# Kernel optimization log

Measured on AMD Instinct MI355X. Metric: run time of the kernel, lower is better.

## Reference

```python
import jax, jax.numpy as jnp
import numpy as np
from jax import lax

B, IN, H, OUT, M, R = 16384, 512, 1024, 512, 8, 256


def setup_inputs() -> dict:
    key = jax.random.key(0)
    ks = jax.random.split(key, 14)
    s = lambda *sh: 1.0 / np.sqrt(sh[-2] if len(sh) > 1 else sh[-1])
    return {
        "x": jax.random.normal(ks[0], (B, IN), jnp.float32),
        "W_in": jax.random.normal(ks[1], (IN, H), jnp.float32) * (1.0 / np.sqrt(IN)),
        "b_in": jnp.zeros((H,), jnp.float32),
        "W_mod": jax.random.normal(ks[2], (M, H, H), jnp.float32) * (1.0 / np.sqrt(H)),
        "b_mod": jnp.zeros((M, H), jnp.float32),
        "Wr1": jax.random.normal(ks[3], (H, R), jnp.float32) * (1.0 / np.sqrt(H)),
        "br1": jnp.zeros((R,), jnp.float32),
        "Wr2": jax.random.normal(ks[4], (R, M), jnp.float32) * (1.0 / np.sqrt(R)),
        "br2": jnp.zeros((M,), jnp.float32),
        "Wc": jax.random.normal(ks[5], (1, H), jnp.float32),
        "bc": jnp.zeros((H,), jnp.float32),
        "W_out": jax.random.normal(ks[6], (H, OUT), jnp.float32) * (1.0 / np.sqrt(H)),
        "b_out": jnp.zeros((OUT,), jnp.float32),
        "max_cycles": 4,
    }


def reference(x, W_in, b_in, W_mod, b_mod, Wr1, br1, Wr2, br2, Wc, bc, W_out, b_out, max_cycles):
    h = x @ W_in + b_in                      # [B, H]
    orig = h

    def body(h, c):
        # cycle_projection: Linear(1, H) applied to scalar cycle index c
        cycle_proj = c * Wc[0] + bc          # [H]
        r = jax.nn.relu((orig * cycle_proj) @ Wr1 + br1)   # [B, R]
        probs = jax.nn.softmax(r @ Wr2 + br2, axis=-1)     # [B, M]
        # all experts as one batched GEMM: [B,H] x [M,H,H] -> [B,M,H]
        expert = jax.nn.relu(jnp.einsum('bh,mhd->bmd', h, W_mod) + b_mod)
        h_new = jnp.einsum('bmd,bm->bd', expert, probs)    # softmax-weighted sum
        return h_new, None

    h, _ = lax.scan(body, h, jnp.arange(max_cycles, dtype=x.dtype))
    return h @ W_out + b_out                 # [B, OUT]
```

## Files before the change

### kernel.cpp

```cpp
#include <hip/hip_runtime.h>


typedef _Float16 half8 __attribute__((ext_vector_type(8)));
typedef _Float16 half4v __attribute__((ext_vector_type(4)));
typedef float floatx4 __attribute__((ext_vector_type(4)));

#define DEVI __device__ __forceinline__

DEVI void async16(void* lds, const void* g) {
  __builtin_amdgcn_global_load_lds(
      (const __attribute__((address_space(1))) unsigned int*)g,
      (__attribute__((address_space(3))) unsigned int*)lds, 16, 0, 0);
}

DEVI floatx4 mfma_f16(half8 a, half8 b, floatx4 c) {
  return __builtin_amdgcn_mfma_f32_16x16x32_f16(a, b, c, 0, 0, 0);
}


__global__ __launch_bounds__(256) void k_cast16(const float* __restrict__ in,
                                                _Float16* __restrict__ o,
                                                int n4) {
  int i = blockIdx.x * 256 + threadIdx.x;
  if (i >= n4) return;
  float4 v = ((const float4*)in)[i];
  half4v h;
  h[0] = (_Float16)v.x;
  h[1] = (_Float16)v.y;
  h[2] = (_Float16)v.z;
  h[3] = (_Float16)v.w;
  ((half4v*)o)[i] = h;
}

__global__ __launch_bounds__(256) void k_transpose16(
    const float* __restrict__ in, const float* __restrict__ scale,
    _Float16* __restrict__ o, int R, int C) {
  __shared__ float tile[64][65];
  __shared__ float srow[64];
  int b = blockIdx.z;
  int r0 = blockIdx.y * 64, c0 = blockIdx.x * 64;
  const float* src = in + (size_t)b * R * C;
  int t = threadIdx.x;
  int lr = t >> 4;
  int lc4 = (t & 15) * 4;
#pragma unroll
  for (int rr = 0; rr < 64; rr += 16) {
    float4 v = *(const float4*)&src[(size_t)(r0 + lr + rr) * C + c0 + lc4];
    tile[lr + rr][lc4 + 0] = v.x;
    tile[lr + rr][lc4 + 1] = v.y;
    tile[lr + rr][lc4 + 2] = v.z;
    tile[lr + rr][lc4 + 3] = v.w;
  }
  if (t < 64) srow[t] = scale ? scale[r0 + t] : 1.0f;
  __syncthreads();
  int oc = t >> 2;
  int orr = (t & 3) * 16;
  alignas(16) _Float16 hv[16];
#pragma unroll
  for (int k = 0; k < 16; k++)
    hv[k] = (_Float16)(tile[orr + k][oc] * srow[orr + k]);
  size_t ob = (size_t)b * C * R + (size_t)(c0 + oc) * R + (r0 + orr);
  ((int4*)&o[ob])[0] = ((int4*)hv)[0];
  ((int4*)&o[ob])[1] = ((int4*)hv)[1];
}


__global__ __launch_bounds__(256) void k_gemm_f16(
    const _Float16* __restrict__ A, const _Float16* __restrict__ Bt,
    const float* __restrict__ bias, _Float16* __restrict__ O, int M, int N,
    int K) {
  __shared__ _Float16 sA[128 * 32], sB[128 * 32];
  int t = threadIdx.x, lane = t & 63, wave = t >> 6;
  int wr = wave >> 1, wc = wave & 1;
  int row0 = blockIdx.y * 128, col0 = blockIdx.x * 128;
  floatx4 acc[4][4];
  for (int i = 0; i < 4; i++)
    for (int j = 0; j < 4; j++) acc[i][j] = (floatx4){0.f, 0.f, 0.f, 0.f};
  int rr0 = t >> 2, kk0 = (t & 3) * 8;
  int ar = (lane & 15) * 32 + (lane >> 4) * 8;
  for (int k0 = 0; k0 < K; k0 += 32) {
    __syncthreads();
    async16(&sA[t * 8], &A[(size_t)(row0 + rr0) * K + k0 + kk0]);
    async16(&sA[(t + 256) * 8], &A[(size_t)(row0 + rr0 + 64) * K + k0 + kk0]);
    async16(&sB[t * 8], &Bt[(size_t)(col0 + rr0) * K + k0 + kk0]);
    async16(&sB[(t + 256) * 8], &Bt[(size_t)(col0 + rr0 + 64) * K + k0 + kk0]);
    __syncthreads();
    half8 a[4], b[4];
#pragma unroll
    for (int i = 0; i < 4; i++) {
      a[i] = *(const half8*)&sA[(wr * 64 + i * 16) * 32 + ar];
      b[i] = *(const half8*)&sB[(wc * 64 + i * 16) * 32 + ar];
    }
#pragma unroll
    for (int i = 0; i < 4; i++)
#pragma unroll
      for (int j = 0; j < 4; j++) acc[i][j] = mfma_f16(a[i], b[j], acc[i][j]);
  }
#pragma unroll
  for (int i = 0; i < 4; i++) {
    int rowb = row0 + wr * 64 + i * 16 + ((lane >> 4) << 2);
#pragma unroll
    for (int j = 0; j < 4; j++) {
      int col = col0 + wc * 64 + j * 16 + (lane & 15);
      float bv = bias ? bias[col] : 0.0f;
#pragma unroll
      for (int r = 0; r < 4; r++)
        O[(size_t)(rowb + r) * N + col] = (_Float16)(acc[i][j][r] + bv);
    }
  }
}

__global__ __launch_bounds__(256) void k_gemm_f32(
    const _Float16* __restrict__ A, const _Float16* __restrict__ Bt,
    const float* __restrict__ bias, float* __restrict__ O, int M, int N,
    int K) {
  __shared__ _Float16 sA[128 * 32], sB[128 * 32];
  int t = threadIdx.x, lane = t & 63, wave = t >> 6;
  int wr = wave >> 1, wc = wave & 1;
  int row0 = blockIdx.y * 128, col0 = blockIdx.x * 128;
  floatx4 acc[4][4];
  for (int i = 0; i < 4; i++)
    for (int j = 0; j < 4; j++) acc[i][j] = (floatx4){0.f, 0.f, 0.f, 0.f};
  int rr0 = t >> 2, kk0 = (t & 3) * 8;
  int ar = (lane & 15) * 32 + (lane >> 4) * 8;
  for (int k0 = 0; k0 < K; k0 += 32) {
    __syncthreads();
    async16(&sA[t * 8], &A[(size_t)(row0 + rr0) * K + k0 + kk0]);
    async16(&sA[(t + 256) * 8], &A[(size_t)(row0 + rr0 + 64) * K + k0 + kk0]);
    async16(&sB[t * 8], &Bt[(size_t)(col0 + rr0) * K + k0 + kk0]);
    async16(&sB[(t + 256) * 8], &Bt[(size_t)(col0 + rr0 + 64) * K + k0 + kk0]);
    __syncthreads();
    half8 a[4], b[4];
#pragma unroll
    for (int i = 0; i < 4; i++) {
      a[i] = *(const half8*)&sA[(wr * 64 + i * 16) * 32 + ar];
      b[i] = *(const half8*)&sB[(wc * 64 + i * 16) * 32 + ar];
    }
#pragma unroll
    for (int i = 0; i < 4; i++)
#pragma unroll
      for (int j = 0; j < 4; j++) acc[i][j] = mfma_f16(a[i], b[j], acc[i][j]);
  }
#pragma unroll
  for (int i = 0; i < 4; i++) {
    int rowb = row0 + wr * 64 + i * 16 + ((lane >> 4) << 2);
#pragma unroll
    for (int j = 0; j < 4; j++) {
      int col = col0 + wc * 64 + j * 16 + (lane & 15);
      float bv = bias ? bias[col] : 0.0f;
#pragma unroll
      for (int r = 0; r < 4; r++)
        O[(size_t)(rowb + r) * N + col] = acc[i][j][r] + bv;
    }
  }
}


__global__ __launch_bounds__(256) void k_router4(
    const float* __restrict__ PQ, const float* __restrict__ br1,
    const float* __restrict__ Wr2, const float* __restrict__ br2,
    float* __restrict__ probs, int B) {
  int lane = threadIdx.x & 63;
  int wave = threadIdx.x >> 6;
  int row = blockIdx.x * 4 + wave;
  float cval = (float)blockIdx.y;
  float4 p4 = ((const float4*)(PQ + (size_t)row * 512))[lane];
  float4 q4 = ((const float4*)(PQ + (size_t)row * 512 + 256))[lane];
  float4 b4 = ((const float4*)br1)[lane];
  float rv[4];
  rv[0] = fmaxf(cval * p4.x + q4.x + b4.x, 0.f);
  rv[1] = fmaxf(cval * p4.y + q4.y + b4.y, 0.f);
  rv[2] = fmaxf(cval * p4.z + q4.z + b4.z, 0.f);
  rv[3] = fmaxf(cval * p4.w + q4.w + b4.w, 0.f);
  float lg[8] = {0.f, 0.f, 0.f, 0.f, 0.f, 0.f, 0.f, 0.f};
#pragma unroll
  for (int k = 0; k < 4; k++) {
    const float4* w = (const float4*)(Wr2 + (size_t)(lane * 4 + k) * 8);
    float4 w0 = w[0], w1 = w[1];
    lg[0] += rv[k] * w0.x;
    lg[1] += rv[k] * w0.y;
    lg[2] += rv[k] * w0.z;
    lg[3] += rv[k] * w0.w;
    lg[4] += rv[k] * w1.x;
    lg[5] += rv[k] * w1.y;
    lg[6] += rv[k] * w1.z;
    lg[7] += rv[k] * w1.w;
  }
#pragma unroll
  for (int s = 32; s > 0; s >>= 1)
#pragma unroll
    for (int m = 0; m < 8; m++) lg[m] += __shfl_xor(lg[m], s);
#pragma unroll
  for (int m = 0; m < 8; m++) lg[m] += br2[m];
  float mx = lg[0];
#pragma unroll
  for (int m = 1; m < 8; m++) mx = fmaxf(mx, lg[m]);
  float e[8];
  float sum = 0.f;
#pragma unroll
  for (int m = 0; m < 8; m++) {
    e[m] = expf(lg[m] - mx);
    sum += e[m];
  }
  float inv = 1.f / sum;
  if (lane < 8)
    probs[(size_t)blockIdx.y * B * 8 + (size_t)row * 8 + lane] = e[lane] * inv;
}


__global__ __launch_bounds__(256) void k_expert_partial(
    const _Float16* __restrict__ hin, const _Float16* __restrict__ WT,
    const float* __restrict__ bmod, const float* __restrict__ probs,
    _Float16* __restrict__ part, int rowbase) {
  __shared__ _Float16 sA[128 * 32];
  __shared__ _Float16 sB[128 * 32];
  __shared__ float sProb[128];
  __shared__ float sBias[128];
  const int K = 1024;
  int t = threadIdx.x, lane = t & 63, wave = t >> 6;
  int wr = wave >> 1, wc = wave & 1;
  int m = blockIdx.z;
  int col0 = blockIdx.x * 128;
  int prow0 = blockIdx.y * 128;
  int grow0 = rowbase + prow0;
  if (t < 128)
    sProb[t] = probs[(size_t)(grow0 + t) * 8 + m];
  else
    sBias[t - 128] = bmod[(size_t)m * 1024 + col0 + (t - 128)];
  const _Float16* Bm = WT + (size_t)m * 1024 * 1024;
  floatx4 acc[4][4];
  for (int i = 0; i < 4; i++)
    for (int j = 0; j < 4; j++) acc[i][j] = (floatx4){0.f, 0.f, 0.f, 0.f};
  int rr0 = t >> 2, kk0 = (t & 3) * 8;
  int ar = (lane & 15) * 32 + (lane >> 4) * 8;
  for (int k0 = 0; k0 < K; k0 += 32) {
    __syncthreads();
    async16(&sA[t * 8], &hin[(size_t)(grow0 + rr0) * K + k0 + kk0]);
    async16(&sA[(t + 256) * 8],
            &hin[(size_t)(grow0 + rr0 + 64) * K + k0 + kk0]);
    async16(&sB[t * 8], &Bm[(size_t)(col0 + rr0) * K + k0 + kk0]);
    async16(&sB[(t + 256) * 8], &Bm[(size_t)(col0 + rr0 + 64) * K + k0 + kk0]);
    __syncthreads();
    half8 a[4], b[4];
#pragma unroll
    for (int i = 0; i < 4; i++) {
      a[i] = *(const half8*)&sA[(wr * 64 + i * 16) * 32 + ar];
      b[i] = *(const half8*)&sB[(wc * 64 + i * 16) * 32 + ar];
    }
#pragma unroll
    for (int i = 0; i < 4; i++)
#pragma unroll
      for (int j = 0; j < 4; j++) acc[i][j] = mfma_f16(a[i], b[j], acc[i][j]);
  }
#pragma unroll
  for (int i = 0; i < 4; i++) {
    int lr0 = wr * 64 + i * 16 + ((lane >> 4) << 2);
    float p0 = sProb[lr0 + 0];
    float p1 = sProb[lr0 + 1];
    float p2 = sProb[lr0 + 2];
    float p3 = sProb[lr0 + 3];
#pragma unroll
    for (int j = 0; j < 4; j++) {
      int cl = wc * 64 + j * 16 + (lane & 15);
      float bb = sBias[cl];
      size_t base =
          (size_t)m * 4096 * 1024 + (size_t)(prow0 + lr0) * 1024 + col0 + cl;
      part[base + 0 * 1024] = (_Float16)(p0 * fmaxf(acc[i][j][0] + bb, 0.f));
      part[base + 1 * 1024] = (_Float16)(p1 * fmaxf(acc[i][j][1] + bb, 0.f));
      part[base + 2 * 1024] = (_Float16)(p2 * fmaxf(acc[i][j][2] + bb, 0.f));
      part[base + 3 * 1024] = (_Float16)(p3 * fmaxf(acc[i][j][3] + bb, 0.f));
    }
  }
}

__global__ __launch_bounds__(256) void k_combine8(
    const _Float16* __restrict__ part, _Float16* __restrict__ hout,
    int rowbase) {
  const size_t S = (size_t)4096 * 1024;
  size_t i = ((size_t)blockIdx.x * 256 + threadIdx.x) * 8;
  float s[8] = {0.f, 0.f, 0.f, 0.f, 0.f, 0.f, 0.f, 0.f};
#pragma unroll
  for (int m = 0; m < 8; m++) {
    half8 v = *(const half8*)&part[(size_t)m * S + i];
#pragma unroll
    for (int k = 0; k < 8; k++) s[k] += (float)v[k];
  }
  half8 o;
#pragma unroll
  for (int k = 0; k < 8; k++) o[k] = (_Float16)s[k];
  *(half8*)&hout[(size_t)rowbase * 1024 + i] = o;
}


extern "C" void kernel_launch(void* const* d_in, const int* in_sizes, int n_in,
                              void* d_out, int out_size, void* d_ws,
                              size_t ws_size, hipStream_t stream) {
  (void)in_sizes;
  (void)n_in;
  (void)out_size;
  (void)ws_size;
  const float* x = (const float*)d_in[0];
  const float* W_in = (const float*)d_in[1];
  const float* b_in = (const float*)d_in[2];
  const float* W_mod = (const float*)d_in[3];
  const float* b_mod = (const float*)d_in[4];
  const float* Wr1 = (const float*)d_in[5];
  const float* br1 = (const float*)d_in[6];
  const float* Wr2 = (const float*)d_in[7];
  const float* br2 = (const float*)d_in[8];
  const float* Wc = (const float*)d_in[9];
  const float* bc = (const float*)d_in[10];
  const float* W_out = (const float*)d_in[11];
  const float* b_out = (const float*)d_in[12];
  float* out = (float*)d_out;

  const int B = 16384, IN = 512, H = 1024, OUT = 512, M = 8, R = 256;
  const size_t MB = 1024 * 1024;

  char* p = (char*)d_ws;
  _Float16* partial = (_Float16*)(p + 0);
  _Float16* xh = (_Float16*)(p + 0);
  _Float16* WinT = (_Float16*)(p + 64 * MB);
  _Float16* W1T = (_Float16*)(p + 65 * MB);
  _Float16* WoutT = (_Float16*)(p + 66 * MB);
  _Float16* WmodT = (_Float16*)(p + 67 * MB);
  _Float16* origHi = (_Float16*)(p + 83 * MB);
  _Float16* hA = (_Float16*)(p + 115 * MB);
  _Float16* hB = (_Float16*)(p + 147 * MB);
  float* PQ = (float*)(p + 179 * MB);
  float* probs4 = (float*)(p + 211 * MB);

  k_cast16<<<dim3(B * IN / 4 / 256), dim3(256), 0, stream>>>(x, xh,
                                                             B * IN / 4);
  k_transpose16<<<dim3(H / 64, IN / 64, 1), dim3(256), 0, stream>>>(
      W_in, nullptr, WinT, IN, H);
  k_transpose16<<<dim3(R / 64, H / 64, 1), dim3(256), 0, stream>>>(
      Wr1, Wc, W1T, H, R);
  k_transpose16<<<dim3(R / 64, H / 64, 1), dim3(256), 0, stream>>>(
      Wr1, bc, W1T + (size_t)R * H, H, R);
  k_transpose16<<<dim3(OUT / 64, H / 64, 1), dim3(256), 0, stream>>>(
      W_out, nullptr, WoutT, H, OUT);
  k_transpose16<<<dim3(H / 64, H / 64, M), dim3(256), 0, stream>>>(
      W_mod, nullptr, WmodT, H, H);

  k_gemm_f16<<<dim3(H / 128, B / 128), dim3(256), 0, stream>>>(
      xh, WinT, b_in, origHi, B, H, IN);
  k_gemm_f32<<<dim3(2 * R / 128, B / 128), dim3(256), 0, stream>>>(
      origHi, W1T, nullptr, PQ, B, 2 * R, H);
  k_router4<<<dim3(B / 4, 4), dim3(256), 0, stream>>>(PQ, br1, Wr2, br2,
                                                      probs4, B);

  const _Float16* hcur = origHi;
  _Float16* hbufs[2] = {hA, hB};
  for (int c = 0; c < 4; c++) {
    const float* probs = probs4 + (size_t)c * B * 8;
    _Float16* hn = hbufs[c & 1];
    for (int chunk = 0; chunk < 4; chunk++) {
      int rowbase = chunk * 4096;
      k_expert_partial<<<dim3(H / 128, 32, M), dim3(256), 0, stream>>>(
          hcur, WmodT, b_mod, probs, partial, rowbase);
      k_combine8<<<dim3(4096 * 1024 / (256 * 8)), dim3(256), 0, stream>>>(
          partial, hn, rowbase);
    }
    hcur = hn;
  }

  k_gemm_f32<<<dim3(OUT / 128, B / 128), dim3(256), 0, stream>>>(
      hcur, WoutT, b_out, out, B, OUT, H);
}
```

Baseline: 1.907 ms.

## Compute expert pairs per block, summing them before writing halved partials

Each block now covers a 256-row tile and two experts (z and z+4) at once. The A tile is loaded once and shared across both experts, and their prob-weighted ReLU outputs are added in registers before one fp16 partial is stored. This halves the partial-buffer writes and the combine reads, and lets the row chunk grow to 8192 with fewer launches. The cost is doubled accumulator register use per thread (512-thread blocks with launch bounds of 2) and more LDS, which may lower occupancy.

```diff
diff --git a/kernel.cpp b/kernel.cpp
--- a/kernel.cpp
+++ b/kernel.cpp
@@ -6,6 +6,7 @@
 typedef float floatx4 __attribute__((ext_vector_type(4)));
 
 #define DEVI __device__ __forceinline__
+#define CHUNK 8192
 
 DEVI void async16(void* lds, const void* g) {
   __builtin_amdgcn_global_load_lds(
@@ -208,79 +209,99 @@
 }
 
 
-__global__ __launch_bounds__(256) void k_expert_partial(
+__global__ __launch_bounds__(512, 2) void k_expert_pair(
     const _Float16* __restrict__ hin, const _Float16* __restrict__ WT,
     const float* __restrict__ bmod, const float* __restrict__ probs,
     _Float16* __restrict__ part, int rowbase) {
-  __shared__ _Float16 sA[128 * 32];
-  __shared__ _Float16 sB[128 * 32];
-  __shared__ float sProb[128];
-  __shared__ float sBias[128];
+  __shared__ _Float16 sA[256 * 32];
+  __shared__ _Float16 sB[2 * 128 * 32];
+  __shared__ float sProb[2 * 256];
+  __shared__ float sBias[2 * 128];
   const int K = 1024;
   int t = threadIdx.x, lane = t & 63, wave = t >> 6;
-  int wr = wave >> 1, wc = wave & 1;
-  int m = blockIdx.z;
+  int wr = wave >> 1;
+  int wc = wave & 1;
+  int z = blockIdx.z;
   int col0 = blockIdx.x * 128;
-  int prow0 = blockIdx.y * 128;
+  int prow0 = blockIdx.y * 256;
   int grow0 = rowbase + prow0;
-  if (t < 128)
-    sProb[t] = probs[(size_t)(grow0 + t) * 8 + m];
-  else
-    sBias[t - 128] = bmod[(size_t)m * 1024 + col0 + (t - 128)];
-  const _Float16* Bm = WT + (size_t)m * 1024 * 1024;
-  floatx4 acc[4][4];
+  if (t < 512) {
+    int e = t >> 8, r = t & 255;
+    sProb[t] = probs[(size_t)(grow0 + r) * 8 + z + e * 4];
+  }
+  if (t < 256) {
+    int e = t >> 7, cc = t & 127;
+    sBias[t] = bmod[(size_t)(z + e * 4) * 1024 + col0 + cc];
+  }
+  const _Float16* B0 = WT + (size_t)z * 1024 * 1024;
+  const _Float16* B1 = WT + (size_t)(z + 4) * 1024 * 1024;
+  floatx4 acc0[4][4], acc1[4][4];
+#pragma unroll
   for (int i = 0; i < 4; i++)
-    for (int j = 0; j < 4; j++) acc[i][j] = (floatx4){0.f, 0.f, 0.f, 0.f};
+#pragma unroll
+    for (int j = 0; j < 4; j++) {
+      acc0[i][j] = (floatx4){0.f, 0.f, 0.f, 0.f};
+      acc1[i][j] = (floatx4){0.f, 0.f, 0.f, 0.f};
+    }
   int rr0 = t >> 2, kk0 = (t & 3) * 8;
   int ar = (lane & 15) * 32 + (lane >> 4) * 8;
   for (int k0 = 0; k0 < K; k0 += 32) {
     __syncthreads();
     async16(&sA[t * 8], &hin[(size_t)(grow0 + rr0) * K + k0 + kk0]);
-    async16(&sA[(t + 256) * 8],
-            &hin[(size_t)(grow0 + rr0 + 64) * K + k0 + kk0]);
-    async16(&sB[t * 8], &Bm[(size_t)(col0 + rr0) * K + k0 + kk0]);
-    async16(&sB[(t + 256) * 8], &Bm[(size_t)(col0 + rr0 + 64) * K + k0 + kk0]);
-    __syncthreads();
-    half8 a[4], b[4];
+    async16(&sA[(t + 512) * 8],
+            &hin[(size_t)(grow0 + rr0 + 128) * K + k0 + kk0]);
+    async16(&sB[t * 8], &B0[(size_t)(col0 + rr0) * K + k0 + kk0]);
+    async16(&sB[(t + 512) * 8], &B1[(size_t)(col0 + rr0) * K + k0 + kk0]);
+    __syncthreads();
+    half8 a[4], b0[4], b1[4];
 #pragma unroll
     for (int i = 0; i < 4; i++) {
       a[i] = *(const half8*)&sA[(wr * 64 + i * 16) * 32 + ar];
-      b[i] = *(const half8*)&sB[(wc * 64 + i * 16) * 32 + ar];
+      b0[i] = *(const half8*)&sB[(wc * 64 + i * 16) * 32 + ar];
+      b1[i] = *(const half8*)&sB[4096 + (wc * 64 + i * 16) * 32 + ar];
     }
 #pragma unroll
     for (int i = 0; i < 4; i++)
 #pragma unroll
-      for (int j = 0; j < 4; j++) acc[i][j] = mfma_f16(a[i], b[j], acc[i][j]);
+      for (int j = 0; j < 4; j++) {
+        acc0[i][j] = mfma_f16(a[i], b0[j], acc0[i][j]);
+        acc1[i][j] = mfma_f16(a[i], b1[j], acc1[i][j]);
+      }
   }
 #pragma unroll
   for (int i = 0; i < 4; i++) {
     int lr0 = wr * 64 + i * 16 + ((lane >> 4) << 2);
-    float p0 = sProb[lr0 + 0];
-    float p1 = sProb[lr0 + 1];
-    float p2 = sProb[lr0 + 2];
-    float p3 = sProb[lr0 + 3];
+    float p0[4], p1[4];
+#pragma unroll
+    for (int r = 0; r < 4; r++) {
+      p0[r] = sProb[lr0 + r];
+      p1[r] = sProb[256 + lr0 + r];
+    }
 #pragma unroll
     for (int j = 0; j < 4; j++) {
       int cl = wc * 64 + j * 16 + (lane & 15);
-      float bb = sBias[cl];
+      float bb0 = sBias[cl];
+      float bb1 = sBias[128 + cl];
       size_t base =
-          (size_t)m * 4096 * 1024 + (size_t)(prow0 + lr0) * 1024 + col0 + cl;
-      part[base + 0 * 1024] = (_Float16)(p0 * fmaxf(acc[i][j][0] + bb, 0.f));
-      part[base + 1 * 1024] = (_Float16)(p1 * fmaxf(acc[i][j][1] + bb, 0.f));
-      part[base + 2 * 1024] = (_Float16)(p2 * fmaxf(acc[i][j][2] + bb, 0.f));
-      part[base + 3 * 1024] = (_Float16)(p3 * fmaxf(acc[i][j][3] + bb, 0.f));
-    }
-  }
-}
-
-__global__ __launch_bounds__(256) void k_combine8(
+          (size_t)z * CHUNK * 1024 + (size_t)(prow0 + lr0) * 1024 + col0 + cl;
+#pragma unroll
+      for (int r = 0; r < 4; r++) {
+        float v = p0[r] * fmaxf(acc0[i][j][r] + bb0, 0.f) +
+                  p1[r] * fmaxf(acc1[i][j][r] + bb1, 0.f);
+        part[base + (size_t)r * 1024] = (_Float16)v;
+      }
+    }
+  }
+}
+
+__global__ __launch_bounds__(256) void k_combine4(
     const _Float16* __restrict__ part, _Float16* __restrict__ hout,
     int rowbase) {
-  const size_t S = (size_t)4096 * 1024;
+  const size_t S = (size_t)CHUNK * 1024;
   size_t i = ((size_t)blockIdx.x * 256 + threadIdx.x) * 8;
   float s[8] = {0.f, 0.f, 0.f, 0.f, 0.f, 0.f, 0.f, 0.f};
 #pragma unroll
-  for (int m = 0; m < 8; m++) {
+  for (int m = 0; m < 4; m++) {
     half8 v = *(const half8*)&part[(size_t)m * S + i];
 #pragma unroll
     for (int k = 0; k < 8; k++) s[k] += (float)v[k];
@@ -355,11 +376,11 @@
   for (int c = 0; c < 4; c++) {
     const float* probs = probs4 + (size_t)c * B * 8;
     _Float16* hn = hbufs[c & 1];
-    for (int chunk = 0; chunk < 4; chunk++) {
-      int rowbase = chunk * 4096;
-      k_expert_partial<<<dim3(H / 128, 32, M), dim3(256), 0, stream>>>(
+    for (int chunk = 0; chunk < 2; chunk++) {
+      int rowbase = chunk * CHUNK;
+      k_expert_pair<<<dim3(H / 128, CHUNK / 256, 4), dim3(512), 0, stream>>>(
           hcur, WmodT, b_mod, probs, partial, rowbase);
-      k_combine8<<<dim3(4096 * 1024 / (256 * 8)), dim3(256), 0, stream>>>(
+      k_combine4<<<dim3(CHUNK * 1024 / (256 * 8)), dim3(256), 0, stream>>>(
           partial, hn, rowbase);
     }
     hcur = hn;
```

Measured after the change: 1.758 ms. 7.8% less time.
